# Performance work log

Hardware: AMD Instinct MI355X
Metric: run time of the kernel (lower is better)

## Reference

```python
import jax, jax.numpy as jnp
import numpy as np

B, S, H, E = 4, 2048, 1024, 8


def setup_inputs() -> dict:
    key = jax.random.key(0)
    k1, k2, k3 = jax.random.split(key, 3)
    scale = 1.0 / np.sqrt(H)
    return {
        "x": jax.random.normal(k1, (B, S, H), dtype=jnp.float32),
        "router_w": jax.random.normal(k2, (H, E), dtype=jnp.float32) * scale,
        "router_b": jnp.zeros((E,), dtype=jnp.float32),
        "expert_w": jax.random.normal(k3, (E, H, H), dtype=jnp.float32) * scale,
        "expert_b": jnp.zeros((E, H), dtype=jnp.float32),
    }


def reference(x, router_w, router_b, expert_w, expert_b):
    # Flatten tokens: [T, H]
    b, s, h = x.shape
    hs = x.reshape(-1, h)
    # Router: logits -> softmax -> top-1 expert (argmax), matching the
    # original forward which routes each token to argmax(softmax(logits)).
    logits = hs @ router_w + router_b                 # [T, E]
    probs = jax.nn.softmax(logits, axis=-1)           # [T, E]
    idx = jnp.argmax(probs, axis=-1)                  # [T]
    gate = jnp.take_along_axis(probs, idx[:, None], axis=-1)  # [T, 1]
    # Per-expert GEMM computed densely for all experts (reference baseline
    # for the sort/dispatch + grouped-GEMM kernel): [T, E, H]
    expert_out = jnp.einsum("th,ehd->ted", hs, expert_w) + expert_b
    # Combine: select routed expert's output, weight by gate value.
    dispatch = jax.nn.one_hot(idx, expert_w.shape[0], dtype=hs.dtype) * gate  # [T, E]
    out = jnp.einsum("te,ted->td", dispatch, expert_out)  # [T, H]
    return out.reshape(b, s, h)
```

## Files before the change

### kernel.cpp

```cpp
#include <hip/hip_runtime.h>

constexpr int kT = 8192;
constexpr int kH = 1024;
constexpr int kE = 8;
constexpr int kMaxTiles = 72;
constexpr int kNS  = 8;
constexpr int kSeg = kH / kNS;
constexpr int kCntStride = 32;

typedef short short8 __attribute__((ext_vector_type(8)));
typedef float floatx4 __attribute__((ext_vector_type(4)));

__device__ inline unsigned short f2b(float f) {
    union { float f; unsigned int u; } v; v.f = f;
    unsigned int r = v.u + 0x7FFFu + ((v.u >> 16) & 1u);
    return (unsigned short)(r >> 16);
}

#define GLDS16(gp, lp)                                                                  \
    __builtin_amdgcn_global_load_lds(                                                   \
        (const __attribute__((address_space(1))) unsigned int*)(gp),                    \
        (__attribute__((address_space(3))) unsigned int*)(lp), 16, 0, 0)

__global__ __launch_bounds__(256) void k_prep(const float* __restrict__ W,
                                              unsigned short* __restrict__ Wt,
                                              const float* __restrict__ x,
                                              unsigned short* __restrict__ xb,
                                              const float* __restrict__ rw,
                                              float* __restrict__ plog,
                                              int* __restrict__ cnt,
                                              int* __restrict__ done) {
    __shared__ __align__(16) char smem[16640];
    int bid = blockIdx.x;
    int tid = threadIdx.x;
    if (bid == 0 && tid < kE + 1) {
        if (tid < kE) cnt[tid * kCntStride] = 0; else *done = 0;
    }
    if (bid < 2048) {
        float (*lds)[65] = (float(*)[65])smem;
        int kb = bid & 15, nb = (bid >> 4) & 15, e = bid >> 8;
        int rr = tid >> 4, c4 = tid & 15;
        const float* Wp = W + ((size_t)e << 20) + (size_t)(kb * 64) * kH + nb * 64;
#pragma unroll
        for (int p = 0; p < 4; ++p) {
            int r = p * 16 + rr;
            float4 v = *(const float4*)(Wp + (size_t)r * kH + c4 * 4);
            lds[r][c4 * 4 + 0] = v.x; lds[r][c4 * 4 + 1] = v.y;
            lds[r][c4 * 4 + 2] = v.z; lds[r][c4 * 4 + 3] = v.w;
        }
        __syncthreads();
        unsigned short* Wo = Wt + ((size_t)e << 20) + (size_t)(nb * 64) * kH + kb * 64;
#pragma unroll
        for (int p = 0; p < 4; ++p) {
            int n = p * 16 + rr;
            ushort4 o;
            o.x = f2b(lds[c4 * 4 + 0][n]);
            o.y = f2b(lds[c4 * 4 + 1][n]);
            o.z = f2b(lds[c4 * 4 + 2][n]);
            o.w = f2b(lds[c4 * 4 + 3][n]);
            *(ushort4*)(Wo + (size_t)n * kH + c4 * 4) = o;
        }
    } else if (bid < 6144) {
        int row = (bid - 2048) * 2 + (tid >> 7);
        int col = (tid & 127) * 8;
        const float* xp = x + (size_t)row * kH + col;
        float4 v0 = *(const float4*)xp;
        float4 v1 = *(const float4*)(xp + 4);
        ushort4 o0, o1;
        o0.x = f2b(v0.x); o0.y = f2b(v0.y); o0.z = f2b(v0.z); o0.w = f2b(v0.w);
        o1.x = f2b(v1.x); o1.y = f2b(v1.y); o1.z = f2b(v1.z); o1.w = f2b(v1.w);
        unsigned short* op = xb + (size_t)row * kH + col;
        *(ushort4*)op = o0;
        *(ushort4*)(op + 4) = o1;
    } else {
        float (*rwT)[132] = (float(*)[132])smem;
        int rbk = bid - 6144;
        int seg = rbk >> 8;
        {
            int hl = tid >> 1, ep = (tid & 1) * 4;
            float4 v = *(const float4*)(rw + (size_t)(seg * kSeg + hl) * kE + ep);
            rwT[ep + 0][hl] = v.x; rwT[ep + 1][hl] = v.y;
            rwT[ep + 2][hl] = v.z; rwT[ep + 3][hl] = v.w;
        }
        __syncthreads();
        int wave = (rbk & 255) * 4 + (tid >> 6);
        int lane = tid & 63;
        int tg = lane >> 3, e = lane & 7;
        int t = wave * 8 + tg;
        const float* xp = x + (size_t)t * kH + seg * kSeg;
        float a0 = 0.f, a1 = 0.f;
#pragma unroll 4
        for (int i = 0; i < kSeg / 8; ++i) {
            float4 xv0 = *(const float4*)(xp + i * 8);
            float4 xv1 = *(const float4*)(xp + i * 8 + 4);
            float4 wv0 = *(const float4*)&rwT[e][i * 8];
            float4 wv1 = *(const float4*)&rwT[e][i * 8 + 4];
            a0 += xv0.x * wv0.x + xv0.y * wv0.y + xv0.z * wv0.z + xv0.w * wv0.w;
            a1 += xv1.x * wv1.x + xv1.y * wv1.y + xv1.z * wv1.z + xv1.w * wv1.w;
        }
        plog[(size_t)t * 64 + e * 8 + seg] = a0 + a1;
    }
}

__global__ __launch_bounds__(256) void k_router_final(const float* __restrict__ plog,
                                                      const float* __restrict__ rb,
                                                      float* __restrict__ gate,
                                                      int* __restrict__ perm2,
                                                      int* __restrict__ cnt,
                                                      int* __restrict__ done,
                                                      int* __restrict__ tile_e,
                                                      int* __restrict__ tile_row) {
    __shared__ int lcnt[kE];
    __shared__ int lbase[kE];
    int tid = threadIdx.x;
    if (tid < kE) lcnt[tid] = 0;
    __syncthreads();

    int wave = blockIdx.x * 4 + (tid >> 6);
    int lane = tid & 63;
    int tg = lane >> 3, e = lane & 7;
    int t = wave * 8 + tg;
    const float* pp = plog + (size_t)t * 64 + e * 8;
    float4 p0 = *(const float4*)pp;
    float4 p1 = *(const float4*)(pp + 4);
    float acc = rb[e] + ((p0.x + p0.y) + (p0.z + p0.w)) + ((p1.x + p1.y) + (p1.z + p1.w));
    float m = acc; int bi = e;
#pragma unroll
    for (int s = 1; s < 8; s <<= 1) {
        float om = __shfl_xor(m, s);
        int   ob = __shfl_xor(bi, s);
        if (om > m || (om == m && ob < bi)) { m = om; bi = ob; }
    }
    float p = __expf(acc - m);
    float sum = p;
#pragma unroll
    for (int s = 1; s < 8; s <<= 1) sum += __shfl_xor(sum, s);

    int lrank = 0;
    if (e == 0) {
        gate[t] = 1.0f / sum;
        lrank = atomicAdd(&lcnt[bi], 1);
    }
    __syncthreads();
    if (tid < kE) lbase[tid] = atomicAdd(&cnt[tid * kCntStride], lcnt[tid]);
    __syncthreads();
    if (e == 0) perm2[bi * kT + lbase[bi] + lrank] = t;

    __syncthreads();
    if (tid == 0) {
        __threadfence();
        int old = atomicAdd(done, 1);
        if (old == (int)gridDim.x - 1) {
            __threadfence();
            int tt = 0;
            for (int ee = 0; ee < kE; ++ee) {
                int c = atomicAdd(&cnt[ee * kCntStride], 0);
                int nt = (c + 127) >> 7;
                for (int i = 0; i < nt; ++i) { tile_e[tt] = ee; tile_row[tt] = i << 7; ++tt; }
            }
            for (; tt < kMaxTiles; ++tt) tile_e[tt] = -1;
        }
    }
}

constexpr int kBK = 64;

__global__ __launch_bounds__(256, 2) void k_gemm(const unsigned short* __restrict__ xb,
                                                 const unsigned short* __restrict__ Wt,
                                                 const float* __restrict__ eb,
                                                 const int* __restrict__ perm2,
                                                 const float* __restrict__ gate,
                                                 const int* __restrict__ cnt,
                                                 const int* __restrict__ tile_e,
                                                 const int* __restrict__ tile_row,
                                                 float* __restrict__ out) {
    int bm = blockIdx.x, bn = blockIdx.y;
    int e = tile_e[bm];
    if (e < 0) return;
    int l0 = tile_row[bm];
    int ce = cnt[e * kCntStride];
    const int* pe = perm2 + e * kT;

    __shared__ __align__(16) unsigned short As[128 * kBK];
    __shared__ __align__(16) unsigned short Bs[128 * kBK];

    int tid = threadIdx.x;
    int wave = tid >> 6, lane = tid & 63;
    int wm = wave & 1, wn = wave >> 1;
    int quad = lane >> 4, l15 = lane & 15;

    floatx4 acc[4][4];
#pragma unroll
    for (int i = 0; i < 4; ++i)
#pragma unroll
        for (int j = 0; j < 4; ++j) acc[i][j] = floatx4{0.f, 0.f, 0.f, 0.f};

    int lrow8 = lane >> 3;
    int lseg8 = (lane & 7) ^ lrow8;
    const unsigned short* aPj[4];
#pragma unroll
    for (int j = 0; j < 4; ++j) {
        int lr = l0 + wave * 32 + j * 8 + lrow8;
        int tok = (lr < ce) ? pe[lr] : 0;
        aPj[j] = xb + (size_t)tok * kH + lseg8 * 8;
    }
    const unsigned short* bP = Wt + ((size_t)e << 20)
                             + (size_t)(bn * 128 + wave * 32 + lrow8) * kH + lseg8 * 8;
    unsigned short* lA = &As[(wave * 32) * kBK];
    unsigned short* lB = &Bs[(wave * 32) * kBK];

    int sw0 = ((0 * 4 + quad) ^ (l15 & 7)) * 8;
    int sw1 = ((1 * 4 + quad) ^ (l15 & 7)) * 8;

    for (int k0 = 0; k0 < kH; k0 += kBK) {
        __syncthreads();
#pragma unroll
        for (int j = 0; j < 4; ++j) {
            GLDS16(aPj[j] + k0, lA + j * 8 * kBK);
            GLDS16(bP + (size_t)(j * 8) * kH + k0, lB + j * 8 * kBK);
        }
        __syncthreads();

        short8 af[4][2], bf[4][2];
#pragma unroll
        for (int i = 0; i < 4; ++i) {
            int r = (wm * 64 + i * 16 + l15) * kBK;
            af[i][0] = *(const short8*)&As[r + sw0];
            af[i][1] = *(const short8*)&As[r + sw1];
        }
#pragma unroll
        for (int i = 0; i < 4; ++i) {
            int r = (wn * 64 + i * 16 + l15) * kBK;
            bf[i][0] = *(const short8*)&Bs[r + sw0];
            bf[i][1] = *(const short8*)&Bs[r + sw1];
        }
#pragma unroll
        for (int ks = 0; ks < 2; ++ks)
#pragma unroll
            for (int i = 0; i < 4; ++i)
#pragma unroll
                for (int j = 0; j < 4; ++j)
                    acc[i][j] = __builtin_amdgcn_mfma_f32_16x16x32_bf16(af[i][ks], bf[j][ks],
                                                                        acc[i][j], 0, 0, 0);
    }

    int colbase = bn * 128 + wn * 64;
#pragma unroll
    for (int i = 0; i < 4; ++i) {
        int rl = l0 + wm * 64 + i * 16 + quad * 4;
#pragma unroll
        for (int rg = 0; rg < 4; ++rg) {
            int lr = rl + rg;
            if (lr >= ce) continue;
            int tok = pe[lr];
            float g = gate[tok];
            float* op = out + (size_t)tok * kH;
#pragma unroll
            for (int j = 0; j < 4; ++j) {
                int col = colbase + j * 16 + l15;
                op[col] = g * (acc[i][j][rg] + eb[e * kH + col]);
            }
        }
    }
}

extern "C" void kernel_launch(void* const* d_in, const int* in_sizes, int n_in,
                              void* d_out, int out_size, void* d_ws, size_t ws_size,
                              hipStream_t stream) {
    const float* x  = (const float*)d_in[0];
    const float* rw = (const float*)d_in[1];
    const float* rb = (const float*)d_in[2];
    const float* ew = (const float*)d_in[3];
    const float* eb = (const float*)d_in[4];
    float* out = (float*)d_out;

    char* p = (char*)d_ws;
    unsigned short* Wt = (unsigned short*)p; p += (size_t)kE * kH * kH * 2;
    unsigned short* xb = (unsigned short*)p; p += (size_t)kT * kH * 2;
    float* plog  = (float*)p; p += (size_t)kT * 64 * 4;
    float* gate  = (float*)p; p += (size_t)kT * 4;
    int* perm2   = (int*)p;   p += (size_t)kE * kT * 4;
    int* cnt     = (int*)p;   p += kE * kCntStride * 4;
    int* done    = (int*)p;   p += 64;
    int* tile_e  = (int*)p;   p += kMaxTiles * 4;
    int* tile_r  = (int*)p;   p += kMaxTiles * 4;

    k_prep<<<8192, 256, 0, stream>>>(ew, Wt, x, xb, rw, plog, cnt, done);
    k_router_final<<<kT / 32, 256, 0, stream>>>(plog, rb, gate, perm2, cnt, done,
                                                tile_e, tile_r);
    dim3 gg(kMaxTiles, kH / 128);
    k_gemm<<<gg, 256, 0, stream>>>(xb, Wt, eb, perm2, gate, cnt, tile_e, tile_r, out);
}
```

Baseline: 167.9 us.

## Fuse router logits, softmax and dispatch into the x-conversion blocks of prep kernel

The router dot products are now computed inside the blocks that convert x to bf16, reusing the loaded x values, so the separate router block range, the partial-logit buffer and the k_router_final kernel are removed. Each block reduces its logits across waves, does the softmax/argmax and scatters tokens through global atomics, and the last of the 4096 finishing blocks builds the tile table. Counter reset moves to a hipMemsetAsync. This saves one kernel launch and a re-read of x, at the cost of per-token global atomics, which make the permutation order nondeterministic, and rw being read from global instead of LDS.

```diff
diff --git a/kernel.cpp b/kernel.cpp
--- a/kernel.cpp
+++ b/kernel.cpp
@@ -4,8 +4,6 @@
 constexpr int kH = 1024;
 constexpr int kE = 8;
 constexpr int kMaxTiles = 72;
-constexpr int kNS  = 8;
-constexpr int kSeg = kH / kNS;
 constexpr int kCntStride = 32;
 
 typedef short short8 __attribute__((ext_vector_type(8)));
@@ -27,17 +25,18 @@
                                               const float* __restrict__ x,
                                               unsigned short* __restrict__ xb,
                                               const float* __restrict__ rw,
-                                              float* __restrict__ plog,
+                                              const float* __restrict__ rb,
+                                              float* __restrict__ gate,
+                                              int* __restrict__ perm2,
                                               int* __restrict__ cnt,
-                                              int* __restrict__ done) {
-    __shared__ __align__(16) char smem[16640];
+                                              int* __restrict__ done,
+                                              int* __restrict__ tile_e,
+                                              int* __restrict__ tile_row) {
+    __shared__ float lds[64][65];
+    __shared__ float red[4][8];
     int bid = blockIdx.x;
     int tid = threadIdx.x;
-    if (bid == 0 && tid < kE + 1) {
-        if (tid < kE) cnt[tid * kCntStride] = 0; else *done = 0;
-    }
     if (bid < 2048) {
-        float (*lds)[65] = (float(*)[65])smem;
         int kb = bid & 15, nb = (bid >> 4) & 15, e = bid >> 8;
         int rr = tid >> 4, c4 = tid & 15;
         const float* Wp = W + ((size_t)e << 20) + (size_t)(kb * 64) * kH + nb * 64;
@@ -60,97 +59,69 @@
             o.w = f2b(lds[c4 * 4 + 3][n]);
             *(ushort4*)(Wo + (size_t)n * kH + c4 * 4) = o;
         }
-    } else if (bid < 6144) {
-        int row = (bid - 2048) * 2 + (tid >> 7);
-        int col = (tid & 127) * 8;
-        const float* xp = x + (size_t)row * kH + col;
-        float4 v0 = *(const float4*)xp;
-        float4 v1 = *(const float4*)(xp + 4);
-        ushort4 o0, o1;
-        o0.x = f2b(v0.x); o0.y = f2b(v0.y); o0.z = f2b(v0.z); o0.w = f2b(v0.w);
-        o1.x = f2b(v1.x); o1.y = f2b(v1.y); o1.z = f2b(v1.z); o1.w = f2b(v1.w);
-        unsigned short* op = xb + (size_t)row * kH + col;
-        *(ushort4*)op = o0;
-        *(ushort4*)(op + 4) = o1;
-    } else {
-        float (*rwT)[132] = (float(*)[132])smem;
-        int rbk = bid - 6144;
-        int seg = rbk >> 8;
-        {
-            int hl = tid >> 1, ep = (tid & 1) * 4;
-            float4 v = *(const float4*)(rw + (size_t)(seg * kSeg + hl) * kE + ep);
-            rwT[ep + 0][hl] = v.x; rwT[ep + 1][hl] = v.y;
-            rwT[ep + 2][hl] = v.z; rwT[ep + 3][hl] = v.w;
-        }
-        __syncthreads();
-        int wave = (rbk & 255) * 4 + (tid >> 6);
-        int lane = tid & 63;
-        int tg = lane >> 3, e = lane & 7;
-        int t = wave * 8 + tg;
-        const float* xp = x + (size_t)t * kH + seg * kSeg;
-        float a0 = 0.f, a1 = 0.f;
-#pragma unroll 4
-        for (int i = 0; i < kSeg / 8; ++i) {
-            float4 xv0 = *(const float4*)(xp + i * 8);
-            float4 xv1 = *(const float4*)(xp + i * 8 + 4);
-            float4 wv0 = *(const float4*)&rwT[e][i * 8];
-            float4 wv1 = *(const float4*)&rwT[e][i * 8 + 4];
-            a0 += xv0.x * wv0.x + xv0.y * wv0.y + xv0.z * wv0.z + xv0.w * wv0.w;
-            a1 += xv1.x * wv1.x + xv1.y * wv1.y + xv1.z * wv1.z + xv1.w * wv1.w;
-        }
-        plog[(size_t)t * 64 + e * 8 + seg] = a0 + a1;
-    }
-}
-
-__global__ __launch_bounds__(256) void k_router_final(const float* __restrict__ plog,
-                                                      const float* __restrict__ rb,
-                                                      float* __restrict__ gate,
-                                                      int* __restrict__ perm2,
-                                                      int* __restrict__ cnt,
-                                                      int* __restrict__ done,
-                                                      int* __restrict__ tile_e,
-                                                      int* __restrict__ tile_row) {
-    __shared__ int lcnt[kE];
-    __shared__ int lbase[kE];
-    int tid = threadIdx.x;
-    if (tid < kE) lcnt[tid] = 0;
+        return;
+    }
+    int rbk = bid - 2048;
+    int row = tid >> 7;
+    int t = rbk * 2 + row;
+    int col = (tid & 127) * 8;
+    const float* xp = x + (size_t)t * kH + col;
+    float4 v0 = *(const float4*)xp;
+    float4 v1 = *(const float4*)(xp + 4);
+    ushort4 o0, o1;
+    o0.x = f2b(v0.x); o0.y = f2b(v0.y); o0.z = f2b(v0.z); o0.w = f2b(v0.w);
+    o1.x = f2b(v1.x); o1.y = f2b(v1.y); o1.z = f2b(v1.z); o1.w = f2b(v1.w);
+    unsigned short* op = xb + (size_t)t * kH + col;
+    *(ushort4*)op = o0;
+    *(ushort4*)(op + 4) = o1;
+
+    float pe[8];
+#pragma unroll
+    for (int e2 = 0; e2 < 8; ++e2) pe[e2] = 0.f;
+#pragma unroll
+    for (int j = 0; j < 8; ++j) {
+        float xv = (j < 4) ? (&v0.x)[j] : (&v1.x)[j - 4];
+        const float* wr = rw + (size_t)(col + j) * kE;
+        float4 w0 = *(const float4*)wr;
+        float4 w1 = *(const float4*)(wr + 4);
+        pe[0] += xv * w0.x; pe[1] += xv * w0.y; pe[2] += xv * w0.z; pe[3] += xv * w0.w;
+        pe[4] += xv * w1.x; pe[5] += xv * w1.y; pe[6] += xv * w1.z; pe[7] += xv * w1.w;
+    }
+#pragma unroll
+    for (int s = 1; s < 64; s <<= 1)
+#pragma unroll
+        for (int e2 = 0; e2 < 8; ++e2) pe[e2] += __shfl_xor(pe[e2], s);
+    int wv = tid >> 6;
+    if ((tid & 63) == 0)
+#pragma unroll
+        for (int e2 = 0; e2 < 8; ++e2) red[wv][e2] = pe[e2];
     __syncthreads();
-
-    int wave = blockIdx.x * 4 + (tid >> 6);
-    int lane = tid & 63;
-    int tg = lane >> 3, e = lane & 7;
-    int t = wave * 8 + tg;
-    const float* pp = plog + (size_t)t * 64 + e * 8;
-    float4 p0 = *(const float4*)pp;
-    float4 p1 = *(const float4*)(pp + 4);
-    float acc = rb[e] + ((p0.x + p0.y) + (p0.z + p0.w)) + ((p1.x + p1.y) + (p1.z + p1.w));
-    float m = acc; int bi = e;
-#pragma unroll
-    for (int s = 1; s < 8; s <<= 1) {
-        float om = __shfl_xor(m, s);
-        int   ob = __shfl_xor(bi, s);
-        if (om > m || (om == m && ob < bi)) { m = om; bi = ob; }
-    }
-    float p = __expf(acc - m);
-    float sum = p;
-#pragma unroll
-    for (int s = 1; s < 8; s <<= 1) sum += __shfl_xor(sum, s);
-
-    int lrank = 0;
-    if (e == 0) {
-        gate[t] = 1.0f / sum;
-        lrank = atomicAdd(&lcnt[bi], 1);
-    }
-    __syncthreads();
-    if (tid < kE) lbase[tid] = atomicAdd(&cnt[tid * kCntStride], lcnt[tid]);
-    __syncthreads();
-    if (e == 0) perm2[bi * kT + lbase[bi] + lrank] = t;
-
+    if (tid < 16) {
+        int rr = tid >> 3, ee = tid & 7;
+        float logit = red[rr * 2][ee] + red[rr * 2 + 1][ee] + rb[ee];
+        float m = logit; int bi = ee;
+#pragma unroll
+        for (int s = 1; s < 8; s <<= 1) {
+            float om = __shfl_xor(m, s);
+            int   ob = __shfl_xor(bi, s);
+            if (om > m || (om == m && ob < bi)) { m = om; bi = ob; }
+        }
+        float p = __expf(logit - m);
+        float sum = p;
+#pragma unroll
+        for (int s = 1; s < 8; s <<= 1) sum += __shfl_xor(sum, s);
+        if (ee == 0) {
+            int tt = rbk * 2 + rr;
+            gate[tt] = 1.0f / sum;
+            int rk = atomicAdd(&cnt[bi * kCntStride], 1);
+            perm2[bi * kT + rk] = tt;
+        }
+    }
     __syncthreads();
     if (tid == 0) {
         __threadfence();
         int old = atomicAdd(done, 1);
-        if (old == (int)gridDim.x - 1) {
+        if (old == 4095) {
             __threadfence();
             int tt = 0;
             for (int ee = 0; ee < kE; ++ee) {
@@ -277,7 +248,6 @@
     char* p = (char*)d_ws;
     unsigned short* Wt = (unsigned short*)p; p += (size_t)kE * kH * kH * 2;
     unsigned short* xb = (unsigned short*)p; p += (size_t)kT * kH * 2;
-    float* plog  = (float*)p; p += (size_t)kT * 64 * 4;
     float* gate  = (float*)p; p += (size_t)kT * 4;
     int* perm2   = (int*)p;   p += (size_t)kE * kT * 4;
     int* cnt     = (int*)p;   p += kE * kCntStride * 4;
@@ -285,9 +255,9 @@
     int* tile_e  = (int*)p;   p += kMaxTiles * 4;
     int* tile_r  = (int*)p;   p += kMaxTiles * 4;
 
-    k_prep<<<8192, 256, 0, stream>>>(ew, Wt, x, xb, rw, plog, cnt, done);
-    k_router_final<<<kT / 32, 256, 0, stream>>>(plog, rb, gate, perm2, cnt, done,
-                                                tile_e, tile_r);
+    hipMemsetAsync(cnt, 0, kE * kCntStride * 4 + 64, stream);
+    k_prep<<<6144, 256, 0, stream>>>(ew, Wt, x, xb, rw, rb, gate, perm2, cnt, done,
+                                     tile_e, tile_r);
     dim3 gg(kMaxTiles, kH / 128);
     k_gemm<<<gg, 256, 0, stream>>>(xb, Wt, eb, perm2, gate, cnt, tile_e, tile_r, out);
 }
```

Result: slower. 309.9 us (+84.6%).
